# Kernel optimization log

Measured on AMD Instinct MI355X. Metric: run time of the kernel, lower is better.

The kernel has to match this reference:

```python
import jax, jax.numpy as jnp
import numpy as np

K_NN = 9
HEADS = 4
SCALE = 2
NUM_CLASSES = 10
BATCH = 256


def pixel_unshuffle(x, s):
    # x: [B, C, H, W] -> [B, C*s*s, H/s, W/s] (torch PixelUnshuffle channel order)
    B, C, H, W = x.shape
    x = x.reshape(B, C, H // s, s, W // s, s)
    return x.transpose(0, 1, 3, 5, 2, 4).reshape(B, C * s * s, H // s, W // s)


def pixel_shuffle(x, s):
    # x: [B, C, H, W] -> [B, C/(s*s), H*s, W*s]
    B, C, H, W = x.shape
    c = C // (s * s)
    x = x.reshape(B, c, s, s, H, W)
    return x.transpose(0, 1, 4, 2, 5, 3).reshape(B, c, H * s, W * s)


def convnn_branch_layer(x, Wc, bc, Wq, Wk, Wv, Wo, bo):
    # Attention_ConvNN_Random_Branching (samples='all', shuffle_pattern='BA'):
    # pixel-unshuffle -> tokens -> [local 1x1-conv branch | KNN attention branch] -> concat -> 1x1 proj -> pixel-shuffle
    x = pixel_unshuffle(x, SCALE)               # [B, Cu, h, w]
    B, Cu, h, w = x.shape
    N = h * w
    t = x.reshape(B, Cu, N).transpose(0, 2, 1)  # [B, N, Cu] tokens

    local = jax.nn.relu(t @ Wc + bc)            # [B, N, r0] local (pointwise) branch

    q = t @ Wq                                  # [B, N, d]
    k = t @ Wk
    v = t @ Wv
    d = q.shape[-1]
    dh = d // HEADS

    # K-nearest-neighbor selection over ALL tokens by q/k similarity
    sim = jnp.einsum('bnd,bmd->bnm', q, k)      # [B, N, N]
    _, idx = jax.lax.top_k(sim, K_NN)           # [B, N, K]

    gather = jax.vmap(lambda a, i: a[i])        # per-batch neighbor gather
    k_nb = gather(k, idx)                       # [B, N, K, d]
    v_nb = gather(v, idx)                       # [B, N, K, d]

    qh = q.reshape(B, N, HEADS, dh)
    k_nbh = k_nb.reshape(B, N, K_NN, HEADS, dh)
    v_nbh = v_nb.reshape(B, N, K_NN, HEADS, dh)

    scale = jnp.asarray(1.0 / np.sqrt(dh), q.dtype)
    logits = jnp.einsum('bnhd,bnkhd->bnhk', qh, k_nbh) * scale  # [B, N, H, K]
    attn = jax.nn.softmax(logits, axis=-1)
    agg = jnp.einsum('bnhk,bnkhd->bnhd', attn, v_nbh).reshape(B, N, d)

    out = jnp.concatenate([local, agg], axis=-1) @ Wo + bo      # [B, N, Co]
    out = out.transpose(0, 2, 1).reshape(B, -1, h, w)
    return pixel_shuffle(out, SCALE)            # [B, out_ch, H, W]


def setup_inputs() -> dict:
    key = jax.random.key(0)
    ks = jax.random.split(key, 20)

    def w(k, shape, fan_in):
        return (jax.random.normal(k, shape, dtype=jnp.float32) / np.sqrt(fan_in)).astype(jnp.float32)

    # layer 1: in_ch=3 -> Cu=12, branches (16,16), out_ch=16 -> Co=64
    Cu1, r1, d1, Co1 = 12, 16, 16, 64
    # layer 2: in_ch=16 -> Cu=64, branches (32,32), out_ch=32 -> Co=128
    Cu2, r2, d2, Co2 = 64, 32, 32, 128

    inp = {
        'x': jax.random.normal(ks[0], (BATCH, 3, 32, 32), dtype=jnp.float32),
        'w1c': w(ks[1], (Cu1, r1), Cu1), 'b1c': jnp.zeros((r1,), jnp.float32),
        'w1q': w(ks[2], (Cu1, d1), Cu1), 'w1k': w(ks[3], (Cu1, d1), Cu1), 'w1v': w(ks[4], (Cu1, d1), Cu1),
        'w1o': w(ks[5], (r1 + d1, Co1), r1 + d1), 'b1o': jnp.zeros((Co1,), jnp.float32),
        'w2c': w(ks[6], (Cu2, r2), Cu2), 'b2c': jnp.zeros((r2,), jnp.float32),
        'w2q': w(ks[7], (Cu2, d2), Cu2), 'w2k': w(ks[8], (Cu2, d2), Cu2), 'w2v': w(ks[9], (Cu2, d2), Cu2),
        'w2o': w(ks[10], (r2 + d2, Co2), r2 + d2), 'b2o': jnp.zeros((Co2,), jnp.float32),
        'fc1_w': w(ks[11], (32768, 1024), 32768), 'fc1_b': jnp.zeros((1024,), jnp.float32),
        'fc2_w': w(ks[12], (1024, NUM_CLASSES), 1024), 'fc2_b': jnp.zeros((NUM_CLASSES,), jnp.float32),
    }
    return inp


def reference(x, w1c, b1c, w1q, w1k, w1v, w1o, b1o,
              w2c, b2c, w2q, w2k, w2v, w2o, b2o,
              fc1_w, fc1_b, fc2_w, fc2_b):
    h = convnn_branch_layer(x, w1c, b1c, w1q, w1k, w1v, w1o, b1o)   # [B, 16, 32, 32]
    h = convnn_branch_layer(h, w2c, b2c, w2q, w2k, w2v, w2o, b2o)   # [B, 32, 32, 32]
    h = h.reshape(h.shape[0], -1)                                   # [B, 32768]
    h = jax.nn.relu(h @ fc1_w + fc1_b)
    return h @ fc2_w + fc2_b                                        # [B, 10]
```

## Files before the change

kernel.cpp:

```cpp
#include <hip/hip_runtime.h>
#include <math.h>


typedef float floatx4 __attribute__((ext_vector_type(4)));
typedef __bf16 bf16x8 __attribute__((ext_vector_type(8)));

static constexpr size_t OQ1 = 0;
static constexpr size_t OK1 = 1048576;
static constexpr size_t OV1 = 2097152;
static constexpr size_t OL1 = 3145728;
static constexpr size_t OA1 = 4194304;
static constexpr size_t OT2 = 5242880;
static constexpr size_t OQ2 = 0;
static constexpr size_t OK2 = 2097152;
static constexpr size_t OV2 = 9437184;
static constexpr size_t OL2 = 11534336;
static constexpr size_t OA2 = 13631488;
static constexpr size_t OH  = 5242880;
static constexpr size_t OPART = 9437184;

__device__ inline bf16x8 pack8(const float* f) {
  bf16x8 v;
#pragma unroll
  for (int i = 0; i < 8; ++i) v[i] = (__bf16)f[i];
  return v;
}

__global__ __launch_bounds__(256) void k1_qkv1(
    const float* __restrict__ x, const float* __restrict__ w1q,
    const float* __restrict__ w1k, const float* __restrict__ w1v,
    const float* __restrict__ w1c, const float* __restrict__ b1c,
    float* __restrict__ q1, float* __restrict__ k1,
    float* __restrict__ v1, float* __restrict__ loc1)
{
  const int tid = threadIdx.x;
  const int slot = tid >> 6;
  const int lane = tid & 63;
  const int tok = blockIdx.x * 4 + slot;
  const int b = tok >> 8, n = tok & 255;
  const int i = n >> 4, j = n & 15;
  __shared__ float ts[4][12];
  if (lane < 12) {
    const int c0 = lane >> 2, si = (lane >> 1) & 1, sj = lane & 1;
    ts[slot][lane] = x[((size_t)(b * 3 + c0) * 32 + 2 * i + si) * 32 + 2 * j + sj];
  }
  __syncthreads();
  const int mat = lane >> 4, col = lane & 15;
  const float* W = (mat == 0) ? w1q : (mat == 1) ? w1k : (mat == 2) ? w1v : w1c;
  float acc = 0.f;
#pragma unroll
  for (int c = 0; c < 12; ++c) acc += ts[slot][c] * W[c * 16 + col];
  const size_t o = (size_t)tok * 16 + col;
  if (mat == 0) q1[o] = acc;
  else if (mat == 1) k1[o] = acc;
  else if (mat == 2) v1[o] = acc;
  else loc1[o] = fmaxf(acc + b1c[col], 0.f);
}

template <int D, int DH, int NH>
__global__ __launch_bounds__(64) void attn_sel(
    const float* __restrict__ q, const float* __restrict__ k,
    const float* __restrict__ v, float* __restrict__ agg)
{
  const int b = blockIdx.x >> 2;
  const int t = (blockIdx.x & 3) * 64 + threadIdx.x;
  __shared__ float ks[256 * D];
  const size_t base = (size_t)b * (256 * D);
  for (int idx = threadIdx.x * 4; idx < 256 * D; idx += 256)
    *(float4*)&ks[idx] = *(const float4*)&k[base + idx];
  float qr[D];
  {
    const float4* qrow = (const float4*)&q[base + (size_t)t * D];
#pragma unroll
    for (int c4 = 0; c4 < D / 4; ++c4) {
      const float4 qv = qrow[c4];
      qr[4 * c4 + 0] = qv.x; qr[4 * c4 + 1] = qv.y;
      qr[4 * c4 + 2] = qv.z; qr[4 * c4 + 3] = qv.w;
    }
  }
  __syncthreads();

  float topv[9];
  int topi[9];
#pragma unroll
  for (int r = 0; r < 9; ++r) { topv[r] = -__builtin_inff(); topi[r] = 0; }

#pragma unroll 2
  for (int m = 0; m < 256; ++m) {
    const float4* kr = (const float4*)&ks[m * D];
    float p0 = 0.f, p1 = 0.f, p2 = 0.f, p3 = 0.f;
#pragma unroll
    for (int g = 0; g < D / 16; ++g) {
      const float4 ka = kr[g * 4 + 0], kb = kr[g * 4 + 1];
      const float4 kc = kr[g * 4 + 2], kd = kr[g * 4 + 3];
      p0 += qr[g*16+ 0]*ka.x + qr[g*16+ 1]*ka.y + qr[g*16+ 2]*ka.z + qr[g*16+ 3]*ka.w;
      p1 += qr[g*16+ 4]*kb.x + qr[g*16+ 5]*kb.y + qr[g*16+ 6]*kb.z + qr[g*16+ 7]*kb.w;
      p2 += qr[g*16+ 8]*kc.x + qr[g*16+ 9]*kc.y + qr[g*16+10]*kc.z + qr[g*16+11]*kc.w;
      p3 += qr[g*16+12]*kd.x + qr[g*16+13]*kd.y + qr[g*16+14]*kd.z + qr[g*16+15]*kd.w;
    }
    const float s = (p0 + p1) + (p2 + p3);
    bool ci = s > topv[8];
#pragma unroll
    for (int i = 8; i >= 1; --i) {
      const bool cim1 = s > topv[i - 1];
      topv[i] = ci ? (cim1 ? topv[i - 1] : s) : topv[i];
      topi[i] = ci ? (cim1 ? topi[i - 1] : m) : topi[i];
      ci = cim1;
    }
    topv[0] = ci ? s : topv[0];
    topi[0] = ci ? m : topi[0];
  }

  const float scale = (DH == 4) ? 0.5f : 0.35355339059327373f;
  float outr[D];
#pragma unroll
  for (int hh = 0; hh < NH; ++hh) {
    float lg9[9];
#pragma unroll
    for (int kk = 0; kk < 9; ++kk) {
      const float4* kr = (const float4*)&k[base + (size_t)topi[kk] * D + hh * DH];
      float s = 0.f;
#pragma unroll
      for (int u = 0; u < DH / 4; ++u) {
        const float4 ka = kr[u];
        s += qr[hh*DH + u*4 + 0]*ka.x + qr[hh*DH + u*4 + 1]*ka.y +
             qr[hh*DH + u*4 + 2]*ka.z + qr[hh*DH + u*4 + 3]*ka.w;
      }
      lg9[kk] = s * scale;
    }
    float mx = lg9[0];
#pragma unroll
    for (int kk = 1; kk < 9; ++kk) mx = fmaxf(mx, lg9[kk]);
    float sum = 0.f;
#pragma unroll
    for (int kk = 0; kk < 9; ++kk) { lg9[kk] = __expf(lg9[kk] - mx); sum += lg9[kk]; }
    const float inv = 1.f / sum;
    float oacc[DH];
#pragma unroll
    for (int c = 0; c < DH; ++c) oacc[c] = 0.f;
#pragma unroll
    for (int kk = 0; kk < 9; ++kk) {
      const float4* vr = (const float4*)&v[base + (size_t)topi[kk] * D + hh * DH];
      const float w = lg9[kk] * inv;
#pragma unroll
      for (int u = 0; u < DH / 4; ++u) {
        const float4 va = vr[u];
        oacc[u*4+0] += w * va.x; oacc[u*4+1] += w * va.y;
        oacc[u*4+2] += w * va.z; oacc[u*4+3] += w * va.w;
      }
    }
#pragma unroll
    for (int c = 0; c < DH; ++c) outr[hh * DH + c] = oacc[c];
  }
  float4* o = (float4*)&agg[base + (size_t)t * D];
#pragma unroll
  for (int c4 = 0; c4 < D / 4; ++c4)
    o[c4] = make_float4(outr[4*c4], outr[4*c4+1], outr[4*c4+2], outr[4*c4+3]);
}

__global__ __launch_bounds__(256) void proj1(
    const float* __restrict__ loc1, const float* __restrict__ agg1,
    const float* __restrict__ w1o, const float* __restrict__ b1o,
    float* __restrict__ t2)
{
  const int tid = threadIdx.x;
  const int tok = blockIdx.x * 256 + tid;
  __shared__ float wS[32 * 64];
  __shared__ float bS[64];
  for (int idx = tid * 4; idx < 2048; idx += 1024)
    *(float4*)&wS[idx] = *(const float4*)&w1o[idx];
  if (tid < 64) bS[tid] = b1o[tid];
  float cat[32];
#pragma unroll
  for (int c4 = 0; c4 < 4; ++c4) {
    const float4 l4 = *(const float4*)&loc1[(size_t)tok * 16 + c4 * 4];
    cat[4*c4+0] = l4.x; cat[4*c4+1] = l4.y; cat[4*c4+2] = l4.z; cat[4*c4+3] = l4.w;
    const float4 a4 = *(const float4*)&agg1[(size_t)tok * 16 + c4 * 4];
    cat[16+4*c4+0] = a4.x; cat[16+4*c4+1] = a4.y; cat[16+4*c4+2] = a4.z; cat[16+4*c4+3] = a4.w;
  }
  __syncthreads();
  float acc[64];
#pragma unroll
  for (int o = 0; o < 64; ++o) acc[o] = 0.f;
#pragma unroll 4
  for (int c = 0; c < 32; ++c) {
    const float cv = cat[c];
#pragma unroll
    for (int o4 = 0; o4 < 16; ++o4) {
      const float4 w4 = *(const float4*)&wS[c * 64 + o4 * 4];
      acc[o4*4+0] += cv * w4.x; acc[o4*4+1] += cv * w4.y;
      acc[o4*4+2] += cv * w4.z; acc[o4*4+3] += cv * w4.w;
    }
  }
  float* dst = t2 + (size_t)tok * 64;
#pragma unroll
  for (int o4 = 0; o4 < 16; ++o4)
    *(float4*)&dst[o4 * 4] = make_float4(acc[o4*4] + bS[o4*4], acc[o4*4+1] + bS[o4*4+1],
                                         acc[o4*4+2] + bS[o4*4+2], acc[o4*4+3] + bS[o4*4+3]);
}

__global__ __launch_bounds__(256) void k4_qkv2(
    const float* __restrict__ t2, const float* __restrict__ w2q,
    const float* __restrict__ w2k, const float* __restrict__ w2v,
    const float* __restrict__ w2c, const float* __restrict__ b2c,
    float* __restrict__ q2, float* __restrict__ k2,
    float* __restrict__ v2, float* __restrict__ loc2)
{
  const int blk = blockIdx.x;
  const int tid = threadIdx.x;
  __shared__ float t2S[64 * 68];
  __shared__ float wS[4 * 2312];
  __shared__ float bS[32];
  for (int idx = tid * 4; idx < 4096; idx += 1024) {
    const float4 vv = *(const float4*)&t2[(size_t)blk * 4096 + idx];
    *(float4*)&t2S[(idx >> 6) * 68 + (idx & 63)] = vv;
  }
  for (int idx = tid * 4; idx < 2048; idx += 1024) {
    const int c = idx >> 5, col = idx & 31;
    *(float4*)&wS[0 * 2312 + c * 36 + col] = *(const float4*)&w2q[idx];
    *(float4*)&wS[1 * 2312 + c * 36 + col] = *(const float4*)&w2k[idx];
    *(float4*)&wS[2 * 2312 + c * 36 + col] = *(const float4*)&w2v[idx];
    *(float4*)&wS[3 * 2312 + c * 36 + col] = *(const float4*)&w2c[idx];
  }
  if (tid < 32) bS[tid] = b2c[tid];
  __syncthreads();
  const int tq = tid >> 2, mat = tid & 3;
  const float* wm = &wS[mat * 2312];
  float acc[32];
#pragma unroll
  for (int e = 0; e < 32; ++e) acc[e] = 0.f;
#pragma unroll 4
  for (int c = 0; c < 64; ++c) {
    const float tv = t2S[tq * 68 + c];
#pragma unroll
    for (int o4 = 0; o4 < 8; ++o4) {
      const float4 w4 = *(const float4*)&wm[c * 36 + o4 * 4];
      acc[o4*4+0] += tv * w4.x; acc[o4*4+1] += tv * w4.y;
      acc[o4*4+2] += tv * w4.z; acc[o4*4+3] += tv * w4.w;
    }
  }
  if (mat == 3) {
#pragma unroll
    for (int e = 0; e < 32; ++e) acc[e] = fmaxf(acc[e] + bS[e], 0.f);
  }
  float* dst = (mat == 0) ? q2 : (mat == 1) ? k2 : (mat == 2) ? v2 : loc2;
  float* drow = dst + (size_t)(blk * 64 + tq) * 32;
#pragma unroll
  for (int o4 = 0; o4 < 8; ++o4)
    *(float4*)&drow[o4 * 4] = make_float4(acc[o4*4], acc[o4*4+1], acc[o4*4+2], acc[o4*4+3]);
}

__global__ __launch_bounds__(256) void proj2h(
    const float* __restrict__ loc2, const float* __restrict__ agg2,
    const float* __restrict__ w2o, const float* __restrict__ b2o,
    __bf16* __restrict__ h)
{
  const int b = blockIdx.x;
  const int t = threadIdx.x;
  __shared__ __bf16 catB[256 * 72];
  __shared__ __bf16 wB[128 * 72];
  {
    const int n = t >> 1, khalf = t & 1;
    float wv[32];
#pragma unroll
    for (int j = 0; j < 32; ++j) wv[j] = w2o[(size_t)(khalf * 32 + j) * 128 + n];
#pragma unroll
    for (int j8 = 0; j8 < 4; ++j8)
      *(bf16x8*)&wB[n * 72 + khalf * 32 + j8 * 8] = pack8(&wv[j8 * 8]);
  }
  {
    float lv[32];
#pragma unroll
    for (int c4 = 0; c4 < 8; ++c4) {
      const float4 x4 = *(const float4*)&loc2[(size_t)(b * 256 + t) * 32 + c4 * 4];
      lv[4*c4+0] = x4.x; lv[4*c4+1] = x4.y; lv[4*c4+2] = x4.z; lv[4*c4+3] = x4.w;
    }
#pragma unroll
    for (int c8 = 0; c8 < 4; ++c8)
      *(bf16x8*)&catB[t * 72 + c8 * 8] = pack8(&lv[c8 * 8]);
#pragma unroll
    for (int c4 = 0; c4 < 8; ++c4) {
      const float4 x4 = *(const float4*)&agg2[(size_t)(b * 256 + t) * 32 + c4 * 4];
      lv[4*c4+0] = x4.x; lv[4*c4+1] = x4.y; lv[4*c4+2] = x4.z; lv[4*c4+3] = x4.w;
    }
#pragma unroll
    for (int c8 = 0; c8 < 4; ++c8)
      *(bf16x8*)&catB[t * 72 + 32 + c8 * 8] = pack8(&lv[c8 * 8]);
  }
  __syncthreads();
  const int w = t >> 6, lane = t & 63, qd = lane >> 4, mcol = lane & 15;
#pragma unroll
  for (int nc = 0; nc < 2; ++nc) {
    floatx4 acc[4][4];
#pragma unroll
    for (int mi = 0; mi < 4; ++mi)
#pragma unroll
      for (int nj = 0; nj < 4; ++nj) acc[mi][nj] = (floatx4)0.f;
#pragma unroll
    for (int s = 0; s < 2; ++s) {
      bf16x8 af[4], bf[4];
#pragma unroll
      for (int mi = 0; mi < 4; ++mi)
        af[mi] = *(const bf16x8*)&catB[(w * 64 + mi * 16 + mcol) * 72 + s * 32 + qd * 8];
#pragma unroll
      for (int nj = 0; nj < 4; ++nj)
        bf[nj] = *(const bf16x8*)&wB[((nc * 4 + nj) * 16 + mcol) * 72 + s * 32 + qd * 8];
#pragma unroll
      for (int mi = 0; mi < 4; ++mi)
#pragma unroll
        for (int nj = 0; nj < 4; ++nj)
          acc[mi][nj] = __builtin_amdgcn_mfma_f32_16x16x32_bf16(af[mi], bf[nj], acc[mi][nj], 0, 0, 0);
    }
#pragma unroll
    for (int mi = 0; mi < 4; ++mi)
#pragma unroll
      for (int nj = 0; nj < 4; ++nj) {
        const int ch = (nc * 4 + nj) * 16 + mcol;
        const float bb = b2o[ch];
        const int cc = ch >> 2, si = (ch >> 1) & 1, sj = ch & 1;
#pragma unroll
        for (int r = 0; r < 4; ++r) {
          const int tok = w * 64 + mi * 16 + qd * 4 + r;
          const int i = tok >> 4, j = tok & 15;
          h[(size_t)b * 32768 + cc * 1024 + (2 * i + si) * 32 + (2 * j + sj)] =
              (__bf16)(acc[mi][nj][r] + bb);
        }
      }
  }
}

__global__ __launch_bounds__(256) void k7_fc1_gemm(
    const __bf16* __restrict__ A,
    const float* __restrict__ Bw,
    float* __restrict__ part)
{
  __shared__ __bf16 Bs[32 * 72];
  const int bn = blockIdx.x & 31;
  const int bm = (blockIdx.x >> 5) & 1;
  const int bk = blockIdx.x >> 6;
  const int n0 = bn * 32, m0 = bm * 128, k0 = bk * 2048;
  const int tid = threadIdx.x;
  const int n = tid & 31, koct = tid >> 5;
  const int w = tid >> 6, lane = tid & 63;
  const int qd = lane >> 4, mcol = lane & 15;
  floatx4 acc[2][2];
#pragma unroll
  for (int mi = 0; mi < 2; ++mi)
#pragma unroll
    for (int ni = 0; ni < 2; ++ni) acc[mi][ni] = (floatx4)0.f;

  for (int it = 0; it < 32; ++it) {
    const int kk0 = k0 + it * 64;
    float bvals[8];
    const float* brow = Bw + (size_t)(kk0 + koct * 8) * 1024 + n0 + n;
#pragma unroll
    for (int j = 0; j < 8; ++j) bvals[j] = brow[(size_t)j * 1024];
    bf16x8 af[2][2];
#pragma unroll
    for (int mi = 0; mi < 2; ++mi)
#pragma unroll
      for (int s = 0; s < 2; ++s)
        af[mi][s] = *(const bf16x8*)(A + (size_t)(m0 + w * 32 + mi * 16 + mcol) * 32768
                                       + kk0 + s * 32 + qd * 8);
    __syncthreads();
    *(bf16x8*)&Bs[n * 72 + koct * 8] = pack8(bvals);
    __syncthreads();
    bf16x8 bf[2][2];
#pragma unroll
    for (int ni = 0; ni < 2; ++ni)
#pragma unroll
      for (int s = 0; s < 2; ++s)
        bf[ni][s] = *(const bf16x8*)&Bs[(ni * 16 + mcol) * 72 + s * 32 + qd * 8];
#pragma unroll
    for (int s = 0; s < 2; ++s)
#pragma unroll
      for (int mi = 0; mi < 2; ++mi)
#pragma unroll
        for (int ni = 0; ni < 2; ++ni)
          acc[mi][ni] = __builtin_amdgcn_mfma_f32_16x16x32_bf16(af[mi][s], bf[ni][s], acc[mi][ni], 0, 0, 0);
  }
  float* P = part + (size_t)bk * 262144;
#pragma unroll
  for (int mi = 0; mi < 2; ++mi)
#pragma unroll
    for (int ni = 0; ni < 2; ++ni) {
      const int col = n0 + ni * 16 + mcol;
#pragma unroll
      for (int r = 0; r < 4; ++r) {
        const int row = m0 + w * 32 + mi * 16 + qd * 4 + r;
        P[(size_t)row * 1024 + col] = acc[mi][ni][r];
      }
    }
}

__global__ __launch_bounds__(256) void k7c8_fc2(
    const float* __restrict__ part, const float* __restrict__ fc1b,
    const float* __restrict__ w2, const float* __restrict__ b2,
    float* __restrict__ out)
{
  const int b = blockIdx.x, t = threadIdx.x;
  const int col4 = t * 4;
  float4 s = make_float4(0.f, 0.f, 0.f, 0.f);
#pragma unroll
  for (int p = 0; p < 16; ++p) {
    const float4 x4 = *(const float4*)&part[(size_t)p * 262144 + (size_t)b * 1024 + col4];
    s.x += x4.x; s.y += x4.y; s.z += x4.z; s.w += x4.w;
  }
  const float4 bb = *(const float4*)&fc1b[col4];
  float a[4] = {fmaxf(s.x + bb.x, 0.f), fmaxf(s.y + bb.y, 0.f),
                fmaxf(s.z + bb.z, 0.f), fmaxf(s.w + bb.w, 0.f)};
  float acc[10];
#pragma unroll
  for (int o = 0; o < 10; ++o) acc[o] = 0.f;
#pragma unroll
  for (int i = 0; i < 4; ++i) {
    const float* wr = w2 + (size_t)(col4 + i) * 10;
#pragma unroll
    for (int o = 0; o < 10; ++o) acc[o] += a[i] * wr[o];
  }
  __shared__ float red[256][10];
#pragma unroll
  for (int o = 0; o < 10; ++o) red[t][o] = acc[o];
  __syncthreads();
  for (int st = 128; st > 0; st >>= 1) {
    if (t < st) {
#pragma unroll
      for (int o = 0; o < 10; ++o) red[t][o] += red[t + st][o];
    }
    __syncthreads();
  }
  if (t < 10) out[b * 10 + t] = red[0][t] + b2[t];
}

extern "C" void kernel_launch(void* const* d_in, const int* in_sizes, int n_in,
                              void* d_out, int out_size, void* d_ws, size_t ws_size,
                              hipStream_t stream)
{
  const float* x    = (const float*)d_in[0];
  const float* w1c  = (const float*)d_in[1];
  const float* b1c  = (const float*)d_in[2];
  const float* w1q  = (const float*)d_in[3];
  const float* w1k  = (const float*)d_in[4];
  const float* w1v  = (const float*)d_in[5];
  const float* w1o  = (const float*)d_in[6];
  const float* b1o  = (const float*)d_in[7];
  const float* w2c  = (const float*)d_in[8];
  const float* b2c  = (const float*)d_in[9];
  const float* w2q  = (const float*)d_in[10];
  const float* w2k  = (const float*)d_in[11];
  const float* w2v  = (const float*)d_in[12];
  const float* w2o  = (const float*)d_in[13];
  const float* b2o  = (const float*)d_in[14];
  const float* fc1w = (const float*)d_in[15];
  const float* fc1b = (const float*)d_in[16];
  const float* fc2w = (const float*)d_in[17];
  const float* fc2b = (const float*)d_in[18];
  float* out = (float*)d_out;
  float* ws = (float*)d_ws;

  float* q1   = ws + OQ1;
  float* k1   = ws + OK1;
  float* v1   = ws + OV1;
  float* loc1 = ws + OL1;
  float* agg1 = ws + OA1;
  float* t2   = ws + OT2;
  float* q2   = ws + OQ2;
  float* k2   = ws + OK2;
  float* v2   = ws + OV2;
  float* loc2 = ws + OL2;
  float* agg2 = ws + OA2;
  __bf16* h   = (__bf16*)(ws + OH);
  float* prt  = ws + OPART;

  k1_qkv1<<<16384, 256, 0, stream>>>(x, w1q, w1k, w1v, w1c, b1c, q1, k1, v1, loc1);
  attn_sel<16, 4, 4><<<1024, 64, 0, stream>>>(q1, k1, v1, agg1);
  proj1<<<256, 256, 0, stream>>>(loc1, agg1, w1o, b1o, t2);
  k4_qkv2<<<1024, 256, 0, stream>>>(t2, w2q, w2k, w2v, w2c, b2c, q2, k2, v2, loc2);
  attn_sel<32, 8, 4><<<1024, 64, 0, stream>>>(q2, k2, v2, agg2);
  proj2h<<<256, 256, 0, stream>>>(loc2, agg2, w2o, b2o, h);
  k7_fc1_gemm<<<1024, 256, 0, stream>>>(h, fc1w, prt);
  k7c8_fc2<<<256, 256, 0, stream>>>(prt, fc1b, fc2w, fc2b, out);
}
```

Before: 582.3 us.

## Split attention top-k scan across four waves and widen fc1 GEMM M-tile

```diff
diff --git a/kernel.cpp b/kernel.cpp
--- a/kernel.cpp
+++ b/kernel.cpp
@@ -58,19 +58,26 @@
 }
 
 template <int D, int DH, int NH>
-__global__ __launch_bounds__(64) void attn_sel(
+__global__ __launch_bounds__(256) void attn_sel(
     const float* __restrict__ q, const float* __restrict__ k,
     const float* __restrict__ v, float* __restrict__ agg)
 {
-  const int b = blockIdx.x >> 2;
-  const int t = (blockIdx.x & 3) * 64 + threadIdx.x;
+  const int blk = blockIdx.x;
+  const int b = blk >> 2;
+  const int t0 = (blk & 3) * 64;
+  const int tid = threadIdx.x;
+  const int tok = tid & 63;
+  const int qt = tid >> 6;
   __shared__ float ks[256 * D];
+  __shared__ float mvS[4 * 576];
+  __shared__ int   miS[4 * 576];
+  __shared__ int   selS[576];
   const size_t base = (size_t)b * (256 * D);
-  for (int idx = threadIdx.x * 4; idx < 256 * D; idx += 256)
+  for (int idx = tid * 4; idx < 256 * D; idx += 1024)
     *(float4*)&ks[idx] = *(const float4*)&k[base + idx];
   float qr[D];
   {
-    const float4* qrow = (const float4*)&q[base + (size_t)t * D];
+    const float4* qrow = (const float4*)&q[base + (size_t)(t0 + tok) * D];
 #pragma unroll
     for (int c4 = 0; c4 < D / 4; ++c4) {
       const float4 qv = qrow[c4];
@@ -86,7 +93,8 @@
   for (int r = 0; r < 9; ++r) { topv[r] = -__builtin_inff(); topi[r] = 0; }
 
 #pragma unroll 2
-  for (int m = 0; m < 256; ++m) {
+  for (int j = 0; j < 64; ++j) {
+    const int m = qt * 64 + j;
     const float4* kr = (const float4*)&ks[m * D];
     float p0 = 0.f, p1 = 0.f, p2 = 0.f, p3 = 0.f;
 #pragma unroll
@@ -110,52 +118,82 @@
     topv[0] = ci ? s : topv[0];
     topi[0] = ci ? m : topi[0];
   }
-
+#pragma unroll
+  for (int r = 0; r < 9; ++r) {
+    mvS[qt * 576 + tok * 9 + r] = topv[r];
+    miS[qt * 576 + tok * 9 + r] = topi[r];
+  }
+  __syncthreads();
+  if (qt == 0) {
+    float fv[9];
+    int fi[9];
+#pragma unroll
+    for (int r = 0; r < 9; ++r) { fv[r] = -__builtin_inff(); fi[r] = 0; }
+#pragma unroll
+    for (int qq = 0; qq < 4; ++qq)
+#pragma unroll
+      for (int r = 0; r < 9; ++r) {
+        const float s = mvS[qq * 576 + tok * 9 + r];
+        const int ix = miS[qq * 576 + tok * 9 + r];
+        bool ci = s > fv[8];
+#pragma unroll
+        for (int i = 8; i >= 1; --i) {
+          const bool cim1 = s > fv[i - 1];
+          fv[i] = ci ? (cim1 ? fv[i - 1] : s) : fv[i];
+          fi[i] = ci ? (cim1 ? fi[i - 1] : ix) : fi[i];
+          ci = cim1;
+        }
+        fv[0] = ci ? s : fv[0];
+        fi[0] = ci ? ix : fi[0];
+      }
+#pragma unroll
+    for (int r = 0; r < 9; ++r) selS[tok * 9 + r] = fi[r];
+  }
+  __syncthreads();
+
+  const int hh = qt;
   const float scale = (DH == 4) ? 0.5f : 0.35355339059327373f;
-  float outr[D];
-#pragma unroll
-  for (int hh = 0; hh < NH; ++hh) {
-    float lg9[9];
-#pragma unroll
-    for (int kk = 0; kk < 9; ++kk) {
-      const float4* kr = (const float4*)&k[base + (size_t)topi[kk] * D + hh * DH];
-      float s = 0.f;
-#pragma unroll
-      for (int u = 0; u < DH / 4; ++u) {
-        const float4 ka = kr[u];
-        s += qr[hh*DH + u*4 + 0]*ka.x + qr[hh*DH + u*4 + 1]*ka.y +
-             qr[hh*DH + u*4 + 2]*ka.z + qr[hh*DH + u*4 + 3]*ka.w;
-      }
-      lg9[kk] = s * scale;
-    }
-    float mx = lg9[0];
-#pragma unroll
-    for (int kk = 1; kk < 9; ++kk) mx = fmaxf(mx, lg9[kk]);
-    float sum = 0.f;
-#pragma unroll
-    for (int kk = 0; kk < 9; ++kk) { lg9[kk] = __expf(lg9[kk] - mx); sum += lg9[kk]; }
-    const float inv = 1.f / sum;
-    float oacc[DH];
-#pragma unroll
-    for (int c = 0; c < DH; ++c) oacc[c] = 0.f;
-#pragma unroll
-    for (int kk = 0; kk < 9; ++kk) {
-      const float4* vr = (const float4*)&v[base + (size_t)topi[kk] * D + hh * DH];
-      const float w = lg9[kk] * inv;
-#pragma unroll
-      for (int u = 0; u < DH / 4; ++u) {
-        const float4 va = vr[u];
-        oacc[u*4+0] += w * va.x; oacc[u*4+1] += w * va.y;
-        oacc[u*4+2] += w * va.z; oacc[u*4+3] += w * va.w;
-      }
-    }
-#pragma unroll
-    for (int c = 0; c < DH; ++c) outr[hh * DH + c] = oacc[c];
-  }
-  float4* o = (float4*)&agg[base + (size_t)t * D];
-#pragma unroll
-  for (int c4 = 0; c4 < D / 4; ++c4)
-    o[c4] = make_float4(outr[4*c4], outr[4*c4+1], outr[4*c4+2], outr[4*c4+3]);
+  int sel9[9];
+#pragma unroll
+  for (int kk = 0; kk < 9; ++kk) sel9[kk] = selS[tok * 9 + kk];
+  float lg9[9];
+#pragma unroll
+  for (int kk = 0; kk < 9; ++kk) {
+    const float4* kr = (const float4*)&k[base + (size_t)sel9[kk] * D + hh * DH];
+    float s = 0.f;
+#pragma unroll
+    for (int u = 0; u < DH / 4; ++u) {
+      const float4 ka = kr[u];
+      s += qr[hh*DH + u*4 + 0]*ka.x + qr[hh*DH + u*4 + 1]*ka.y +
+           qr[hh*DH + u*4 + 2]*ka.z + qr[hh*DH + u*4 + 3]*ka.w;
+    }
+    lg9[kk] = s * scale;
+  }
+  float mx = lg9[0];
+#pragma unroll
+  for (int kk = 1; kk < 9; ++kk) mx = fmaxf(mx, lg9[kk]);
+  float sum = 0.f;
+#pragma unroll
+  for (int kk = 0; kk < 9; ++kk) { lg9[kk] = __expf(lg9[kk] - mx); sum += lg9[kk]; }
+  const float inv = 1.f / sum;
+  float oacc[DH];
+#pragma unroll
+  for (int c = 0; c < DH; ++c) oacc[c] = 0.f;
+#pragma unroll
+  for (int kk = 0; kk < 9; ++kk) {
+    const float4* vr = (const float4*)&v[base + (size_t)sel9[kk] * D + hh * DH];
+    const float w = lg9[kk] * inv;
+#pragma unroll
+    for (int u = 0; u < DH / 4; ++u) {
+      const float4 va = vr[u];
+      oacc[u*4+0] += w * va.x; oacc[u*4+1] += w * va.y;
+      oacc[u*4+2] += w * va.z; oacc[u*4+3] += w * va.w;
+    }
+  }
+  float* o = &agg[base + (size_t)(t0 + tok) * D + hh * DH];
+#pragma unroll
+  for (int u = 0; u < DH / 4; ++u)
+    *(float4*)&o[u * 4] = make_float4(oacc[u*4], oacc[u*4+1], oacc[u*4+2], oacc[u*4+3]);
 }
 
 __global__ __launch_bounds__(256) void proj1(
@@ -336,16 +374,15 @@
 {
   __shared__ __bf16 Bs[32 * 72];
   const int bn = blockIdx.x & 31;
-  const int bm = (blockIdx.x >> 5) & 1;
-  const int bk = blockIdx.x >> 6;
-  const int n0 = bn * 32, m0 = bm * 128, k0 = bk * 2048;
+  const int bk = blockIdx.x >> 5;
+  const int n0 = bn * 32, k0 = bk * 2048;
   const int tid = threadIdx.x;
   const int n = tid & 31, koct = tid >> 5;
   const int w = tid >> 6, lane = tid & 63;
   const int qd = lane >> 4, mcol = lane & 15;
-  floatx4 acc[2][2];
-#pragma unroll
-  for (int mi = 0; mi < 2; ++mi)
+  floatx4 acc[4][2];
+#pragma unroll
+  for (int mi = 0; mi < 4; ++mi)
 #pragma unroll
     for (int ni = 0; ni < 2; ++ni) acc[mi][ni] = (floatx4)0.f;
 
@@ -355,12 +392,12 @@
     const float* brow = Bw + (size_t)(kk0 + koct * 8) * 1024 + n0 + n;
 #pragma unroll
     for (int j = 0; j < 8; ++j) bvals[j] = brow[(size_t)j * 1024];
-    bf16x8 af[2][2];
-#pragma unroll
-    for (int mi = 0; mi < 2; ++mi)
+    bf16x8 af[4][2];
+#pragma unroll
+    for (int mi = 0; mi < 4; ++mi)
 #pragma unroll
       for (int s = 0; s < 2; ++s)
-        af[mi][s] = *(const bf16x8*)(A + (size_t)(m0 + w * 32 + mi * 16 + mcol) * 32768
+        af[mi][s] = *(const bf16x8*)(A + (size_t)(w * 64 + mi * 16 + mcol) * 32768
                                        + kk0 + s * 32 + qd * 8);
     __syncthreads();
     *(bf16x8*)&Bs[n * 72 + koct * 8] = pack8(bvals);
@@ -374,20 +411,20 @@
 #pragma unroll
     for (int s = 0; s < 2; ++s)
 #pragma unroll
-      for (int mi = 0; mi < 2; ++mi)
+      for (int mi = 0; mi < 4; ++mi)
 #pragma unroll
         for (int ni = 0; ni < 2; ++ni)
           acc[mi][ni] = __builtin_amdgcn_mfma_f32_16x16x32_bf16(af[mi][s], bf[ni][s], acc[mi][ni], 0, 0, 0);
   }
   float* P = part + (size_t)bk * 262144;
 #pragma unroll
-  for (int mi = 0; mi < 2; ++mi)
+  for (int mi = 0; mi < 4; ++mi)
 #pragma unroll
     for (int ni = 0; ni < 2; ++ni) {
       const int col = n0 + ni * 16 + mcol;
 #pragma unroll
       for (int r = 0; r < 4; ++r) {
-        const int row = m0 + w * 32 + mi * 16 + qd * 4 + r;
+        const int row = w * 64 + mi * 16 + qd * 4 + r;
         P[(size_t)row * 1024 + col] = acc[mi][ni][r];
       }
     }
@@ -473,11 +510,11 @@
   float* prt  = ws + OPART;
 
   k1_qkv1<<<16384, 256, 0, stream>>>(x, w1q, w1k, w1v, w1c, b1c, q1, k1, v1, loc1);
-  attn_sel<16, 4, 4><<<1024, 64, 0, stream>>>(q1, k1, v1, agg1);
+  attn_sel<16, 4, 4><<<1024, 256, 0, stream>>>(q1, k1, v1, agg1);
   proj1<<<256, 256, 0, stream>>>(loc1, agg1, w1o, b1o, t2);
   k4_qkv2<<<1024, 256, 0, stream>>>(t2, w2q, w2k, w2v, w2c, b2c, q2, k2, v2, loc2);
-  attn_sel<32, 8, 4><<<1024, 64, 0, stream>>>(q2, k2, v2, agg2);
+  attn_sel<32, 8, 4><<<1024, 256, 0, stream>>>(q2, k2, v2, agg2);
   proj2h<<<256, 256, 0, stream>>>(loc2, agg2, w2o, b2o, h);
-  k7_fc1_gemm<<<1024, 256, 0, stream>>>(h, fc1w, prt);
+  k7_fc1_gemm<<<512, 256, 0, stream>>>(h, fc1w, prt);
   k7c8_fc2<<<256, 256, 0, stream>>>(prt, fc1b, fc2w, fc2b, out);
 }
```

Measured after the change: 473.6 us. 1.23x faster.
